# Optimization experiments

Measured on AMD Instinct MI355X. Metric: run time of the kernel, lower is better.

Reference implementation:

```python
import jax, jax.numpy as jnp
import numpy as np

DIM = 512
DIM_EDGES = 64
LN_EPS = 1e-5


def setup_inputs() -> dict:
    key = jax.random.key(0)
    ks = jax.random.split(key, 4)
    b, n = 2, 768
    x = jax.random.normal(ks[0], (b, n, DIM), dtype=jnp.float32)
    # nn.Linear weights stored as [out, in], applied as x @ W.T
    W_rows = jax.random.normal(ks[1], (DIM_EDGES, DIM), dtype=jnp.float32) / np.sqrt(DIM)
    W_cols = jax.random.normal(ks[2], (DIM_EDGES, DIM), dtype=jnp.float32) / np.sqrt(DIM)
    W_edges = jax.random.normal(ks[3], (DIM_EDGES, DIM_EDGES), dtype=jnp.float32) / np.sqrt(DIM_EDGES)
    ln_gamma = jnp.ones((DIM_EDGES,), dtype=jnp.float32)
    ln_beta = jnp.zeros((DIM_EDGES,), dtype=jnp.float32)
    return {"x": x, "W_rows": W_rows, "W_cols": W_cols, "W_edges": W_edges,
            "ln_gamma": ln_gamma, "ln_beta": ln_beta}


def reference(x, W_rows, W_cols, W_edges, ln_gamma, ln_beta):
    # rows/cols: [b, n, d_e]
    rows = jnp.einsum('bnd,ed->bne', x, W_rows)
    cols = jnp.einsum('bnd,ed->bne', x, W_cols)
    # outer sum: [b, i, j, d_e]
    outer = rows[:, :, None, :] + cols[:, None, :, :]
    # edge linear (no bias): [b, i, j, d_e]
    h = jnp.einsum('bije,fe->bijf', outer, W_edges)
    # LayerNorm over last dim
    mu = jnp.mean(h, axis=-1, keepdims=True)
    var = jnp.mean(jnp.square(h - mu), axis=-1, keepdims=True)
    out = (h - mu) * jax.lax.rsqrt(var + LN_EPS) * ln_gamma + ln_beta
    return out
```

## Files before the change

kernel.cpp:

```cpp
#include <hip/hip_runtime.h>

#define B 2
#define N 768
#define DIM 512
#define DE 64
#define LN_EPS 1e-5f

typedef float f32x4 __attribute__((ext_vector_type(4)));

#define OFF_RC   0
#define OFF_CC   (B*N*DE)
#define OFF_SSR  (2*B*N*DE)
#define OFF_SSC  (2*B*N*DE + B*N)

__global__ __launch_bounds__(256) void ee_precompute(
    const float* __restrict__ x, const float* __restrict__ Wr,
    const float* __restrict__ Wc, const float* __restrict__ We,
    float* __restrict__ Rc, float* __restrict__ Cc,
    float* __restrict__ ssqR, float* __restrict__ ssqC)
{
    __shared__ float xs[DIM];
    __shared__ float rc[2 * DE];

    const int tok = blockIdx.x;
    const int tid = threadIdx.x;
    const int lane = tid & 63;
    const int wave = tid >> 6;

    const float* xp = x + (size_t)tok * DIM;
    xs[tid]       = xp[tid];
    xs[tid + 256] = xp[tid + 256];
    __syncthreads();

    const float4 b0 = *(const float4*)(xs + lane * 8);
    const float4 b1 = *(const float4*)(xs + lane * 8 + 4);
    for (int m = 0; m < 32; ++m) {
        const int o = wave * 32 + m;
        const float* W = (o < DE) ? (Wr + (size_t)o * DIM)
                                  : (Wc + (size_t)(o - DE) * DIM);
        const float4 a0 = *(const float4*)(W + lane * 8);
        const float4 a1 = *(const float4*)(W + lane * 8 + 4);
        float p = a0.x*b0.x + a0.y*b0.y + a0.z*b0.z + a0.w*b0.w
                + a1.x*b1.x + a1.y*b1.y + a1.z*b1.z + a1.w*b1.w;
        #pragma unroll
        for (int s = 1; s < 64; s <<= 1) p += __shfl_xor(p, s);
        if (lane == 0) rc[o] = p;
    }
    __syncthreads();

    if (tid < 128) {
        const int f = lane;
        const float* W = We + (size_t)f * DE;
        const float* rcp = (wave == 0) ? rc : (rc + DE);
        float acc = 0.f;
        #pragma unroll
        for (int e4 = 0; e4 < DE / 4; ++e4) {
            const float4 w4 = *(const float4*)(W + e4 * 4);
            const float4 r4 = *(const float4*)(rcp + e4 * 4);
            acc += w4.x*r4.x + w4.y*r4.y + w4.z*r4.z + w4.w*r4.w;
        }
        float mu = acc;
        #pragma unroll
        for (int s = 1; s < 64; s <<= 1) mu += __shfl_xor(mu, s);
        mu *= (1.f / DE);
        const float c = acc - mu;
        float sq = c * c;
        #pragma unroll
        for (int s = 1; s < 64; s <<= 1) sq += __shfl_xor(sq, s);
        float* dst = ((wave == 0) ? Rc : Cc) + (size_t)tok * DE;
        dst[f] = c;
        if (lane == 0) ((wave == 0) ? ssqR : ssqC)[tok] = sq;
    }
}

__global__ __launch_bounds__(256) void ee_outer_ln(
    const float* __restrict__ Rc, const float* __restrict__ Cc,
    const float* __restrict__ ssqRp, const float* __restrict__ ssqCp,
    const float* __restrict__ gamma, const float* __restrict__ beta,
    float* __restrict__ out)
{
    __shared__ float rs[DE];
    __shared__ float sj[N];

    const int bi = blockIdx.x;
    const int tid = threadIdx.x;
    const int lane = tid & 63;
    const int wave = tid >> 6;
    const int jsub = lane >> 4;
    const int fb = (lane & 15) * 4;

    const int b = bi / N;
    const float* Ccb   = Cc + (size_t)b * N * DE;
    const float* ssqCb = ssqCp + (size_t)b * N;
    float* outb = out + (size_t)bi * N * DE;

    if (tid < DE) rs[tid] = Rc[(size_t)bi * DE + tid];
    __syncthreads();

    const float ssqR = ssqRp[bi];

    #pragma unroll
    for (int jt = 0; jt < N / 256; ++jt) {
        const int j0 = jt * 256 + tid;
        const float* cj = Ccb + (size_t)j0 * DE;
        f32x4 a = (f32x4)(0.f);
        #pragma unroll
        for (int e = 0; e < DE / 4; ++e) {
            const f32x4 w = *(const f32x4*)(rs + e * 4);
            const f32x4 c = *(const f32x4*)(cj + e * 4);
            a += w * c;
        }
        const float p = a.x + a.y + a.z + a.w;
        const float var = (ssqR + ssqCb[j0] + 2.f * p) * (1.f / DE);
        sj[j0] = rsqrtf(var + LN_EPS);
    }
    __syncthreads();

    const f32x4 r  = *(const f32x4*)(rs + fb);
    const f32x4 g  = *(const f32x4*)(gamma + fb);
    const f32x4 be = *(const f32x4*)(beta + fb);

    #pragma unroll 4
    for (int t = 0; t < N / 16; ++t) {
        const int j = t * 16 + wave * 4 + jsub;
        const f32x4 c = *(const f32x4*)(Ccb + (size_t)j * DE + fb);
        const float s = sj[j];
        f32x4 o = (r + c) * (s * g) + be;
        __builtin_nontemporal_store(o, (f32x4*)(outb + (size_t)j * DE + fb));
    }
}

extern "C" void kernel_launch(void* const* d_in, const int* in_sizes, int n_in,
                              void* d_out, int out_size, void* d_ws, size_t ws_size,
                              hipStream_t stream) {
    const float* x     = (const float*)d_in[0];
    const float* Wr    = (const float*)d_in[1];
    const float* Wc    = (const float*)d_in[2];
    const float* We    = (const float*)d_in[3];
    const float* gamma = (const float*)d_in[4];
    const float* beta  = (const float*)d_in[5];
    float* out = (float*)d_out;
    float* ws  = (float*)d_ws;

    float* Rc   = ws + OFF_RC;
    float* Cc   = ws + OFF_CC;
    float* ssqR = ws + OFF_SSR;
    float* ssqC = ws + OFF_SSC;

    ee_precompute<<<B * N, 256, 0, stream>>>(x, Wr, Wc, We, Rc, Cc, ssqR, ssqC);
    ee_outer_ln<<<B * N, 256, 0, stream>>>(Rc, Cc, ssqR, ssqC, gamma, beta, out);
}
```

Measured before the change: 357.6 us.

## Fuse row projection into outer-LN kernel and process two tokens per column block

Moves the row projection, edge linear and centering for each row token into the output kernel, so the Rc/ssqR workspace round trip is gone. The column precompute kernel now handles two tokens per block, reusing each Wc row load for both. The output is a 2*768*768*64 fp32 tensor, so the output kernel is bound by its stores and the moved row work adds little relative to that. The first kernel shrinks, but the overall effect is likely small.

```diff
diff --git a/kernel.cpp b/kernel.cpp
--- a/kernel.cpp
+++ b/kernel.cpp
@@ -8,55 +8,62 @@
 
 typedef float f32x4 __attribute__((ext_vector_type(4)));
 
-#define OFF_RC   0
-#define OFF_CC   (B*N*DE)
-#define OFF_SSR  (2*B*N*DE)
-#define OFF_SSC  (2*B*N*DE + B*N)
+#define OFF_CC   0
+#define OFF_SSC  (B*N*DE)
 
-__global__ __launch_bounds__(256) void ee_precompute(
-    const float* __restrict__ x, const float* __restrict__ Wr,
-    const float* __restrict__ Wc, const float* __restrict__ We,
-    float* __restrict__ Rc, float* __restrict__ Cc,
-    float* __restrict__ ssqR, float* __restrict__ ssqC)
+__global__ __launch_bounds__(256) void ee_cols(
+    const float* __restrict__ x, const float* __restrict__ Wc,
+    const float* __restrict__ We,
+    float* __restrict__ Cc, float* __restrict__ ssqC)
 {
-    __shared__ float xs[DIM];
-    __shared__ float rc[2 * DE];
+    __shared__ float xs[2 * DIM];
+    __shared__ float cc[2 * DE];
 
-    const int tok = blockIdx.x;
+    const int tok0 = blockIdx.x * 2;
     const int tid = threadIdx.x;
     const int lane = tid & 63;
     const int wave = tid >> 6;
 
-    const float* xp = x + (size_t)tok * DIM;
+    const float* xp = x + (size_t)tok0 * DIM;
     xs[tid]       = xp[tid];
     xs[tid + 256] = xp[tid + 256];
+    xs[tid + 512] = xp[tid + 512];
+    xs[tid + 768] = xp[tid + 768];
     __syncthreads();
 
-    const float4 b0 = *(const float4*)(xs + lane * 8);
-    const float4 b1 = *(const float4*)(xs + lane * 8 + 4);
-    for (int m = 0; m < 32; ++m) {
-        const int o = wave * 32 + m;
-        const float* W = (o < DE) ? (Wr + (size_t)o * DIM)
-                                  : (Wc + (size_t)(o - DE) * DIM);
+    const float4 b00 = *(const float4*)(xs + lane * 8);
+    const float4 b01 = *(const float4*)(xs + lane * 8 + 4);
+    const float4 b10 = *(const float4*)(xs + DIM + lane * 8);
+    const float4 b11 = *(const float4*)(xs + DIM + lane * 8 + 4);
+
+    for (int m = 0; m < 16; ++m) {
+        const int f = wave * 16 + m;
+        const float* W = Wc + (size_t)f * DIM;
         const float4 a0 = *(const float4*)(W + lane * 8);
         const float4 a1 = *(const float4*)(W + lane * 8 + 4);
-        float p = a0.x*b0.x + a0.y*b0.y + a0.z*b0.z + a0.w*b0.w
-                + a1.x*b1.x + a1.y*b1.y + a1.z*b1.z + a1.w*b1.w;
+        float p0 = a0.x*b00.x + a0.y*b00.y + a0.z*b00.z + a0.w*b00.w
+                 + a1.x*b01.x + a1.y*b01.y + a1.z*b01.z + a1.w*b01.w;
+        float p1 = a0.x*b10.x + a0.y*b10.y + a0.z*b10.z + a0.w*b10.w
+                 + a1.x*b11.x + a1.y*b11.y + a1.z*b11.z + a1.w*b11.w;
         #pragma unroll
-        for (int s = 1; s < 64; s <<= 1) p += __shfl_xor(p, s);
-        if (lane == 0) rc[o] = p;
+        for (int s = 1; s < 64; s <<= 1) {
+            p0 += __shfl_xor(p0, s);
+            p1 += __shfl_xor(p1, s);
+        }
+        if (lane == 0) { cc[f] = p0; cc[DE + f] = p1; }
     }
     __syncthreads();
 
     if (tid < 128) {
+        const int t = wave;
         const int f = lane;
         const float* W = We + (size_t)f * DE;
-        const float* rcp = (wave == 0) ? rc : (rc + DE);
+        const float* ccp = cc + t * DE;
         float acc = 0.f;
         #pragma unroll
         for (int e4 = 0; e4 < DE / 4; ++e4) {
             const float4 w4 = *(const float4*)(W + e4 * 4);
-            const float4 r4 = *(const float4*)(rcp + e4 * 4);
+            const float4 r4 = *(const float4*)(ccp + e4 * 4);
             acc += w4.x*r4.x + w4.y*r4.y + w4.z*r4.z + w4.w*r4.w;
         }
         float mu = acc;
@@ -67,20 +74,23 @@
         float sq = c * c;
         #pragma unroll
         for (int s = 1; s < 64; s <<= 1) sq += __shfl_xor(sq, s);
-        float* dst = ((wave == 0) ? Rc : Cc) + (size_t)tok * DE;
-        dst[f] = c;
-        if (lane == 0) ((wave == 0) ? ssqR : ssqC)[tok] = sq;
+        Cc[(size_t)(tok0 + t) * DE + f] = c;
+        if (lane == 0) ssqC[tok0 + t] = sq;
     }
 }
 
-__global__ __launch_bounds__(256) void ee_outer_ln(
-    const float* __restrict__ Rc, const float* __restrict__ Cc,
-    const float* __restrict__ ssqRp, const float* __restrict__ ssqCp,
+__global__ __launch_bounds__(256) void ee_rows_ln(
+    const float* __restrict__ x, const float* __restrict__ Wr,
+    const float* __restrict__ We,
+    const float* __restrict__ Cc, const float* __restrict__ ssqCp,
     const float* __restrict__ gamma, const float* __restrict__ beta,
     float* __restrict__ out)
 {
+    __shared__ float xs[DIM];
+    __shared__ float rr[DE];
     __shared__ float rs[DE];
     __shared__ float sj[N];
+    __shared__ float ssqR_s;
 
     const int bi = blockIdx.x;
     const int tid = threadIdx.x;
@@ -94,10 +104,49 @@
     const float* ssqCb = ssqCp + (size_t)b * N;
     float* outb = out + (size_t)bi * N * DE;
 
-    if (tid < DE) rs[tid] = Rc[(size_t)bi * DE + tid];
+    const float* xp = x + (size_t)bi * DIM;
+    xs[tid]       = xp[tid];
+    xs[tid + 256] = xp[tid + 256];
     __syncthreads();
 
-    const float ssqR = ssqRp[bi];
+    const float4 b0 = *(const float4*)(xs + lane * 8);
+    const float4 b1 = *(const float4*)(xs + lane * 8 + 4);
+    for (int m = 0; m < 16; ++m) {
+        const int o = wave * 16 + m;
+        const float* W = Wr + (size_t)o * DIM;
+        const float4 a0 = *(const float4*)(W + lane * 8);
+        const float4 a1 = *(const float4*)(W + lane * 8 + 4);
+        float p = a0.x*b0.x + a0.y*b0.y + a0.z*b0.z + a0.w*b0.w
+                + a1.x*b1.x + a1.y*b1.y + a1.z*b1.z + a1.w*b1.w;
+        #pragma unroll
+        for (int s = 1; s < 64; s <<= 1) p += __shfl_xor(p, s);
+        if (lane == 0) rr[o] = p;
+    }
+    __syncthreads();
+
+    if (tid < 64) {
+        const float* W = We + (size_t)tid * DE;
+        float acc = 0.f;
+        #pragma unroll
+        for (int e4 = 0; e4 < DE / 4; ++e4) {
+            const float4 w4 = *(const float4*)(W + e4 * 4);
+            const float4 r4 = *(const float4*)(rr + e4 * 4);
+            acc += w4.x*r4.x + w4.y*r4.y + w4.z*r4.z + w4.w*r4.w;
+        }
+        float mu = acc;
+        #pragma unroll
+        for (int s = 1; s < 64; s <<= 1) mu += __shfl_xor(mu, s);
+        mu *= (1.f / DE);
+        const float c = acc - mu;
+        float sq = c * c;
+        #pragma unroll
+        for (int s = 1; s < 64; s <<= 1) sq += __shfl_xor(sq, s);
+        rs[tid] = c;
+        if (tid == 0) ssqR_s = sq;
+    }
+    __syncthreads();
+
+    const float ssqR = ssqR_s;
 
     #pragma unroll
     for (int jt = 0; jt < N / 256; ++jt) {
@@ -142,11 +191,9 @@
     float* out = (float*)d_out;
     float* ws  = (float*)d_ws;
 
-    float* Rc   = ws + OFF_RC;
     float* Cc   = ws + OFF_CC;
-    float* ssqR = ws + OFF_SSR;
     float* ssqC = ws + OFF_SSC;
 
-    ee_precompute<<<B * N, 256, 0, stream>>>(x, Wr, Wc, We, Rc, Cc, ssqR, ssqC);
-    ee_outer_ln<<<B * N, 256, 0, stream>>>(Rc, Cc, ssqR, ssqC, gamma, beta, out);
+    ee_cols<<<B * N / 2, 256, 0, stream>>>(x, Wc, We, Cc, ssqC);
+    ee_rows_ln<<<B * N, 256, 0, stream>>>(x, Wr, We, Cc, ssqC, gamma, beta, out);
 }
```

Result: no change. 359.0 us (+0.4%).
